# Kernel optimization log

Hardware: AMD Instinct MI355X
Metric: run time of the kernel (lower is better)

The kernel has to match this reference:

```python
import jax, jax.numpy as jnp
import numpy as np

HIDDEN = 768


def _rotary(x):
    # x: [B, S, H]; matches torch sinusoidal_position_embedding + rotary math
    B, S, H = x.shape
    pos = jnp.arange(S, dtype=jnp.float32)[:, None]            # [S, 1]
    inv_freq = jnp.power(10000.0, -2.0 * jnp.arange(H // 2, dtype=jnp.float32) / H)
    ang = pos * inv_freq                                       # [S, H/2]
    cos = jnp.repeat(jnp.cos(ang), 2, axis=-1)                 # cos_pos = pos_emb[...,1::2] repeated
    sin = jnp.repeat(jnp.sin(ang), 2, axis=-1)                 # sin_pos = pos_emb[...,::2] repeated
    x_rot = jnp.stack([-x[..., 1::2], x[..., ::2]], axis=-1).reshape(x.shape)
    return x * cos + x_rot * sin


def setup_inputs() -> dict:
    key = jax.random.key(0)
    k1, k2, k3, k4 = jax.random.split(key, 4)
    B, N, M, H = 4, 128, 128, HIDDEN
    review = jax.random.normal(k1, (B, N, H), dtype=jnp.float32)
    reply = jax.random.normal(k2, (B, M, H), dtype=jnp.float32)
    # nn.Linear(2H, H): weight [H, 2H], bias [H]
    bound = 1.0 / np.sqrt(2 * H)
    W = jax.random.uniform(k3, (H, 2 * H), dtype=jnp.float32, minval=-bound, maxval=bound)
    b = jax.random.uniform(k4, (H,), dtype=jnp.float32, minval=-bound, maxval=bound)
    return {"review": review, "reply": reply, "W": W, "b": b}


def reference(review, reply, W, b):
    # rotary position embedding on both inputs
    review = _rotary(review)   # [B, N, H]
    reply = _rotary(reply)     # [B, M, H]
    H = review.shape[-1]
    # Linear on concat([review, reply]) == review @ W_r^T + reply @ W_p^T + b
    W_r, W_p = W[:, :H], W[:, H:]                         # each [H, H]
    proj_review = jnp.einsum('bnh,oh->bno', review, W_r)  # [B, N, H]
    proj_reply = jnp.einsum('bmh,oh->bmo', reply, W_p)    # [B, M, H]
    out = proj_review[:, :, None, :] + proj_reply[:, None, :, :] + b  # [B, N, M, H]
    return jax.nn.relu(out)
```

## Files before the change

### kernel.cpp

```cpp
#include <hip/hip_runtime.h>

#define HID   768
#define BATCH 4
#define SEQ   128
#define NROWS 512
#define PAIRS_PER_MAT (NROWS * (HID/2))

typedef __bf16 bf16x8 __attribute__((ext_vector_type(8)));
typedef float  floatx4 __attribute__((ext_vector_type(4)));

__device__ __forceinline__ unsigned short f2bf(float x) {
    unsigned u = __builtin_bit_cast(unsigned, x);
    unsigned r = u + 0x7FFFu + ((u >> 16) & 1u);
    return (unsigned short)(r >> 16);
}

__global__ __launch_bounds__(256) void rotary_kernel(
    const float* __restrict__ review,
    const float* __restrict__ reply,
    unsigned short* __restrict__ rot)
{
    int p   = blockIdx.x * 256 + threadIdx.x;
    int mat = (p >= PAIRS_PER_MAT) ? 1 : 0;
    int rem = p - mat * PAIRS_PER_MAT;
    int row = rem / (HID / 2);
    int i   = rem - row * (HID / 2);
    int s   = row & 127;

    const float* src = (mat ? reply : review) + row * HID + 2 * i;
    float2 x = *reinterpret_cast<const float2*>(src);

    float inv = exp2f(-(float)i * (13.287712379549449f / 384.0f));
    float ang = (float)s * inv;
    float c  = cosf(ang);
    float sn = sinf(ang);

    float oe = x.x * c - x.y * sn;
    float oo = x.y * c + x.x * sn;
    unsigned pk = (unsigned)f2bf(oe) | ((unsigned)f2bf(oo) << 16);
    *reinterpret_cast<unsigned*>(rot + (size_t)mat * (NROWS * HID) + row * HID + 2 * i) = pk;
}

__global__ __launch_bounds__(256) void gemm_kernel(
    const unsigned short* __restrict__ rot,
    const float* __restrict__ W,
    float* __restrict__ proj)
{
    __shared__ __align__(16) unsigned short As[64 * 32];
    __shared__ __align__(16) unsigned short Bs[64 * 32];

    const int tid  = threadIdx.x;
    const int lane = tid & 63;
    const int wave = tid >> 6;
    const int mat  = blockIdx.z;
    const int row0 = blockIdx.y * 64;
    const int col0 = blockIdx.x * 64;
    const int q    = lane >> 4;
    const int r16  = lane & 15;

    const unsigned short* Abase = rot + (size_t)mat * (NROWS * HID);
    const int srow  = tid >> 2;
    const int skoff = (tid & 3) * 8;

    floatx4 acc[4];
#pragma unroll
    for (int c = 0; c < 4; ++c) acc[c] = (floatx4)0.0f;

    for (int k0 = 0; k0 < HID; k0 += 32) {
        __syncthreads();
        *reinterpret_cast<uint4*>(&As[srow * 32 + skoff]) =
            *reinterpret_cast<const uint4*>(&Abase[(row0 + srow) * HID + k0 + skoff]);
        {
            const float* wp = W + (size_t)(col0 + srow) * (2 * HID) + mat * HID + k0 + skoff;
            float4 w0 = *reinterpret_cast<const float4*>(wp);
            float4 w1 = *reinterpret_cast<const float4*>(wp + 4);
            uint4 pk;
            pk.x = (unsigned)f2bf(w0.x) | ((unsigned)f2bf(w0.y) << 16);
            pk.y = (unsigned)f2bf(w0.z) | ((unsigned)f2bf(w0.w) << 16);
            pk.z = (unsigned)f2bf(w1.x) | ((unsigned)f2bf(w1.y) << 16);
            pk.w = (unsigned)f2bf(w1.z) | ((unsigned)f2bf(w1.w) << 16);
            *reinterpret_cast<uint4*>(&Bs[srow * 32 + skoff]) = pk;
        }
        __syncthreads();

        bf16x8 af = *reinterpret_cast<const bf16x8*>(&As[(wave * 16 + r16) * 32 + q * 8]);
#pragma unroll
        for (int c = 0; c < 4; ++c) {
            bf16x8 bf = *reinterpret_cast<const bf16x8*>(&Bs[(c * 16 + r16) * 32 + q * 8]);
            acc[c] = __builtin_amdgcn_mfma_f32_16x16x32_bf16(af, bf, acc[c], 0, 0, 0);
        }
    }

    float* pbase = proj + (size_t)mat * (NROWS * HID);
#pragma unroll
    for (int c = 0; c < 4; ++c) {
        int col = col0 + c * 16 + r16;
#pragma unroll
        for (int rg = 0; rg < 4; ++rg) {
            int row = row0 + wave * 16 + q * 4 + rg;
            pbase[row * HID + col] = acc[c][rg];
        }
    }
}

__global__ __launch_bounds__(256) void bcast_kernel(
    const float* __restrict__ proj,
    const float* __restrict__ bias,
    float* __restrict__ out)
{
    const int bn    = blockIdx.x;
    const int chunk = blockIdx.y;
    const int b     = bn >> 7;

    __shared__ __align__(16) float prb[HID];
    const float* pr  = proj + (size_t)bn * HID;
    const float* ppb = proj + (size_t)(NROWS + b * SEQ + chunk * 16) * HID;
    for (int o = threadIdx.x; o < HID; o += 256)
        prb[o] = pr[o] + bias[o];
    __syncthreads();

    float* obase = out + (size_t)bn * (SEQ * HID) + (size_t)chunk * 16 * HID;
#pragma unroll 4
    for (int it = 0; it < 12; ++it) {
        int idx = it * 256 + threadIdx.x;
        int m   = idx / 192;
        int t   = idx - m * 192;
        int o4  = t * 4;

        floatx4 p = *reinterpret_cast<const floatx4*>(ppb + m * HID + o4);
        floatx4 a = *reinterpret_cast<const floatx4*>(&prb[o4]);
        floatx4 r;
        r.x = fmaxf(a.x + p.x, 0.0f);
        r.y = fmaxf(a.y + p.y, 0.0f);
        r.z = fmaxf(a.z + p.z, 0.0f);
        r.w = fmaxf(a.w + p.w, 0.0f);
        __builtin_nontemporal_store(r, reinterpret_cast<floatx4*>(obase + m * HID + o4));
    }
}

extern "C" void kernel_launch(void* const* d_in, const int* in_sizes, int n_in,
                              void* d_out, int out_size, void* d_ws, size_t ws_size,
                              hipStream_t stream) {
    const float* review = (const float*)d_in[0];
    const float* reply  = (const float*)d_in[1];
    const float* W      = (const float*)d_in[2];
    const float* bias   = (const float*)d_in[3];
    float* out = (float*)d_out;

    unsigned short* rot = (unsigned short*)d_ws;
    float* proj = (float*)((char*)d_ws + (size_t)2 * NROWS * HID * sizeof(unsigned short));

    rotary_kernel<<<PAIRS_PER_MAT * 2 / 256, 256, 0, stream>>>(review, reply, rot);
    dim3 g2(HID / 64, NROWS / 64, 2);
    gemm_kernel<<<g2, 256, 0, stream>>>(rot, W, proj);
    dim3 g3(NROWS, 8);
    bcast_kernel<<<g3, 256, 0, stream>>>(proj, bias, out);
}
```

Measured before the change: 244.6 us.

## Fuse rotary embedding into GEMM A-tile load and use regular output stores

Removes the separate rotary kernel and applies the rotary rotation and bf16 packing while loading each A tile into shared memory in the GEMM. This drops one launch and the round trip of the bf16 intermediate through memory. The cost is recomputing sin/cos for each of the 12 column blocks, now with the fast __sincosf intrinsic, which is less accurate at larger angles. It also switches the broadcast kernel's output writes from nontemporal to ordinary stores.

```diff
diff --git a/kernel.cpp b/kernel.cpp
--- a/kernel.cpp
+++ b/kernel.cpp
@@ -4,7 +4,6 @@
 #define BATCH 4
 #define SEQ   128
 #define NROWS 512
-#define PAIRS_PER_MAT (NROWS * (HID/2))
 
 typedef __bf16 bf16x8 __attribute__((ext_vector_type(8)));
 typedef float  floatx4 __attribute__((ext_vector_type(4)));
@@ -15,34 +14,19 @@
     return (unsigned short)(r >> 16);
 }
 
-__global__ __launch_bounds__(256) void rotary_kernel(
+__device__ __forceinline__ unsigned rotpair(float xe, float xo, float fi, float sf) {
+    float inv = exp2f(fi * (-13.287712379549449f / 384.0f));
+    float ang = sf * inv;
+    float sn, c;
+    __sincosf(ang, &sn, &c);
+    float oe = xe * c - xo * sn;
+    float oo = xo * c + xe * sn;
+    return (unsigned)f2bf(oe) | ((unsigned)f2bf(oo) << 16);
+}
+
+__global__ __launch_bounds__(256) void gemmrot_kernel(
     const float* __restrict__ review,
     const float* __restrict__ reply,
-    unsigned short* __restrict__ rot)
-{
-    int p   = blockIdx.x * 256 + threadIdx.x;
-    int mat = (p >= PAIRS_PER_MAT) ? 1 : 0;
-    int rem = p - mat * PAIRS_PER_MAT;
-    int row = rem / (HID / 2);
-    int i   = rem - row * (HID / 2);
-    int s   = row & 127;
-
-    const float* src = (mat ? reply : review) + row * HID + 2 * i;
-    float2 x = *reinterpret_cast<const float2*>(src);
-
-    float inv = exp2f(-(float)i * (13.287712379549449f / 384.0f));
-    float ang = (float)s * inv;
-    float c  = cosf(ang);
-    float sn = sinf(ang);
-
-    float oe = x.x * c - x.y * sn;
-    float oo = x.y * c + x.x * sn;
-    unsigned pk = (unsigned)f2bf(oe) | ((unsigned)f2bf(oo) << 16);
-    *reinterpret_cast<unsigned*>(rot + (size_t)mat * (NROWS * HID) + row * HID + 2 * i) = pk;
-}
-
-__global__ __launch_bounds__(256) void gemm_kernel(
-    const unsigned short* __restrict__ rot,
     const float* __restrict__ W,
     float* __restrict__ proj)
 {
@@ -58,9 +42,10 @@
     const int q    = lane >> 4;
     const int r16  = lane & 15;
 
-    const unsigned short* Abase = rot + (size_t)mat * (NROWS * HID);
+    const float* act = (mat ? reply : review);
     const int srow  = tid >> 2;
     const int skoff = (tid & 3) * 8;
+    const float sf  = (float)((row0 + srow) & 127);
 
     floatx4 acc[4];
 #pragma unroll
@@ -68,8 +53,18 @@
 
     for (int k0 = 0; k0 < HID; k0 += 32) {
         __syncthreads();
-        *reinterpret_cast<uint4*>(&As[srow * 32 + skoff]) =
-            *reinterpret_cast<const uint4*>(&Abase[(row0 + srow) * HID + k0 + skoff]);
+        {
+            const float* ap = act + (size_t)(row0 + srow) * HID + k0 + skoff;
+            float4 a0 = *reinterpret_cast<const float4*>(ap);
+            float4 a1 = *reinterpret_cast<const float4*>(ap + 4);
+            float fib = (float)((k0 + skoff) >> 1);
+            uint4 pk;
+            pk.x = rotpair(a0.x, a0.y, fib + 0.0f, sf);
+            pk.y = rotpair(a0.z, a0.w, fib + 1.0f, sf);
+            pk.z = rotpair(a1.x, a1.y, fib + 2.0f, sf);
+            pk.w = rotpair(a1.z, a1.w, fib + 3.0f, sf);
+            *reinterpret_cast<uint4*>(&As[srow * 32 + skoff]) = pk;
+        }
         {
             const float* wp = W + (size_t)(col0 + srow) * (2 * HID) + mat * HID + k0 + skoff;
             float4 w0 = *reinterpret_cast<const float4*>(wp);
@@ -134,7 +129,7 @@
         r.y = fmaxf(a.y + p.y, 0.0f);
         r.z = fmaxf(a.z + p.z, 0.0f);
         r.w = fmaxf(a.w + p.w, 0.0f);
-        __builtin_nontemporal_store(r, reinterpret_cast<floatx4*>(obase + m * HID + o4));
+        *reinterpret_cast<floatx4*>(obase + m * HID + o4) = r;
     }
 }
 
@@ -147,12 +142,10 @@
     const float* bias   = (const float*)d_in[3];
     float* out = (float*)d_out;
 
-    unsigned short* rot = (unsigned short*)d_ws;
-    float* proj = (float*)((char*)d_ws + (size_t)2 * NROWS * HID * sizeof(unsigned short));
+    float* proj = (float*)d_ws;
 
-    rotary_kernel<<<PAIRS_PER_MAT * 2 / 256, 256, 0, stream>>>(review, reply, rot);
-    dim3 g2(HID / 64, NROWS / 64, 2);
-    gemm_kernel<<<g2, 256, 0, stream>>>(rot, W, proj);
-    dim3 g3(NROWS, 8);
-    bcast_kernel<<<g3, 256, 0, stream>>>(proj, bias, out);
+    dim3 g1(HID / 64, NROWS / 64, 2);
+    gemmrot_kernel<<<g1, 256, 0, stream>>>(review, reply, W, proj);
+    dim3 g2(NROWS, 8);
+    bcast_kernel<<<g2, 256, 0, stream>>>(proj, bias, out);
 }
```

New measurement: 238.1 us. -2.6%, faster.
